# Kernel tuning notes

Measured on AMD Instinct MI355X. Metric: run time of the kernel, lower is better.

The kernel has to match this reference:

```python
import jax, jax.numpy as jnp
import numpy as np

# model_grid_shape (flipped ensemble grid, all equal here); E = 8 experts
GRID = (2, 2, 2)
E = GRID[0] * GRID[1] * GRID[2]
N = 524288   # query points
H = 64       # sub-model MLP hidden width


def setup_inputs() -> dict:
    key = jax.random.key(0)
    ks = jax.random.split(key, 4)
    # query coordinates in [-1, 1]^3
    x = jax.random.uniform(ks[0], (N, 3), jnp.float32, -1.0, 1.0)
    # per-expert spatial extents: axis-aligned cells tiling [-1,1]^3, in the
    # same flat order as the routing index i0 + i1*g0 + i2*g0*g1
    i = np.arange(E)
    cell = np.stack([i % GRID[0], (i // GRID[0]) % GRID[1],
                     i // (GRID[0] * GRID[1])], axis=-1).astype(np.float32)
    g = np.array(GRID, np.float32)
    extents_min = jnp.asarray(-1.0 + 2.0 * cell / g)          # [E, 3]
    extents_max = jnp.asarray(-1.0 + 2.0 * (cell + 1.0) / g)  # [E, 3]
    # per-expert SRN MLP parameters: 3 -> H -> H -> 1
    W1 = jax.random.normal(ks[1], (E, 3, H), jnp.float32) / np.sqrt(3.0)
    b1 = jnp.zeros((E, H), jnp.float32)
    W2 = jax.random.normal(ks[2], (E, H, H), jnp.float32) / np.sqrt(float(H))
    b2 = jnp.zeros((E, H), jnp.float32)
    W3 = jax.random.normal(ks[3], (E, H, 1), jnp.float32) / np.sqrt(float(H))
    b3 = jnp.zeros((E, 1), jnp.float32)
    return {"x": x, "extents_min": extents_min, "extents_max": extents_max,
            "W1": W1, "b1": b1, "W2": W2, "b2": b2, "W3": W3, "b3": b3}


def reference(x, extents_min, extents_max, W1, b1, W2, b2, W3, b3):
    # --- routing: flat expert index per point (matches torch forward) ---
    u = jnp.clip((x + 1.0) * 0.5, 0.0, 0.99)
    gvec = jnp.asarray(GRID, x.dtype)
    gi = (u * gvec).astype(jnp.int32)                       # [N, 3]
    idx = gi[:, 0] + gi[:, 1] * GRID[0] + gi[:, 2] * (GRID[0] * GRID[1])

    # --- dispatch/combine: scan over experts, masked scatter into y ---
    def body(y, args):
        i, emin, emax, w1, bb1, w2, bb2, w3, bb3 = args
        # normalize point into expert-local [-1, 1]^3
        xn = -1.0 + 2.0 * ((x - emin) / (emax - emin))      # [N, 3]
        h = jax.nn.relu(xn @ w1 + bb1)                      # [N, H]
        h = jax.nn.relu(h @ w2 + bb2)                       # [N, H]
        o = h @ w3 + bb3                                    # [N, 1]
        mask = (idx == i)[:, None]
        return jnp.where(mask, o, y), None

    y0 = jnp.zeros((x.shape[0], 1), x.dtype)
    y, _ = jax.lax.scan(
        body, y0,
        (jnp.arange(E), extents_min, extents_max, W1, b1, W2, b2, W3, b3))
    return y
```

## Files before the change

kernel.cpp:

```cpp
#include <hip/hip_runtime.h>

typedef __bf16 bf16x8 __attribute__((ext_vector_type(8)));
typedef float f32x4 __attribute__((ext_vector_type(4)));
typedef unsigned short u16x8 __attribute__((ext_vector_type(8)));

#define N_PTS 524288
#define HBLK 256
#define PTS_PER_HBLK 2048

__device__ __forceinline__ unsigned short f2bf(float f) {
    unsigned u = __float_as_uint(f);
    u += 0x7FFFu + ((u >> 16) & 1u);
    return (unsigned short)(u >> 16);
}

__device__ __forceinline__ int route(float x0, float x1, float x2) {
    int g0 = (int)(fminf(fmaxf((x0 + 1.0f) * 0.5f, 0.0f), 0.99f) * 2.0f);
    int g1 = (int)(fminf(fmaxf((x1 + 1.0f) * 0.5f, 0.0f), 0.99f) * 2.0f);
    int g2 = (int)(fminf(fmaxf((x2 + 1.0f) * 0.5f, 0.0f), 0.99f) * 2.0f);
    return g0 + 2*g1 + 4*g2;
}

#define OFF_HIST  0u
#define OFF_BB    8192u
#define OFF_CNT   16384u
#define OFF_BASE  16416u
#define OFF_W1P   16448u
#define OFF_W2T   24640u
#define OFF_XG    90176u

extern "C" __global__ void __launch_bounds__(256) k1_hist(
        const float* __restrict__ x, int* __restrict__ hist) {
    __shared__ int lh[8];
    int t = threadIdx.x;
    if (t < 8) lh[t] = 0;
    __syncthreads();
    int base = blockIdx.x * PTS_PER_HBLK;
    #pragma unroll
    for (int i = 0; i < 8; ++i) {
        int p = base + i * 256 + t;
        float x0 = x[3*p], x1 = x[3*p+1], x2 = x[3*p+2];
        atomicAdd(&lh[route(x0, x1, x2)], 1);
    }
    __syncthreads();
    if (t < 8) hist[blockIdx.x * 8 + t] = lh[t];
}

extern "C" __global__ void __launch_bounds__(256) k2_prep(
        const float* __restrict__ emin, const float* __restrict__ emax,
        const float* __restrict__ W1, const float* __restrict__ b1,
        const float* __restrict__ W2,
        const int* __restrict__ hist, int* __restrict__ blockBase,
        int* __restrict__ counts, int* __restrict__ bases,
        float4* __restrict__ W1p, unsigned short* __restrict__ W2T) {
    int t = threadIdx.x;
    if (blockIdx.x == 8) {
        __shared__ int lh[256][9];
        int c[8], incl[8];
        #pragma unroll
        for (int e = 0; e < 8; ++e) { c[e] = hist[t*8 + e]; incl[e] = c[e]; lh[t][e] = c[e]; }
        for (int off = 1; off < 256; off <<= 1) {
            __syncthreads();
            int add[8];
            if (t >= off) {
                #pragma unroll
                for (int e = 0; e < 8; ++e) add[e] = lh[t - off][e];
            }
            __syncthreads();
            if (t >= off) {
                #pragma unroll
                for (int e = 0; e < 8; ++e) { incl[e] += add[e]; lh[t][e] = incl[e]; }
            }
        }
        __syncthreads();
        int tot[8], base[8];
        int r = 0;
        #pragma unroll
        for (int e = 0; e < 8; ++e) { tot[e] = lh[255][e]; base[e] = r; r += tot[e]; }
        #pragma unroll
        for (int e = 0; e < 8; ++e) blockBase[t*8 + e] = base[e] + incl[e] - c[e];
        if (t == 0) {
            #pragma unroll
            for (int e = 0; e < 8; ++e) { counts[e] = tot[e]; bases[e] = base[e]; }
        }
    } else {
        int e = blockIdx.x;
        if (t < 64) {
            int n = t;
            float d0 = emax[e*3+0] - emin[e*3+0];
            float d1 = emax[e*3+1] - emin[e*3+1];
            float d2 = emax[e*3+2] - emin[e*3+2];
            float a0 = 2.0f/d0, a1 = 2.0f/d1, a2 = 2.0f/d2;
            float c0 = -1.0f - 2.0f*emin[e*3+0]/d0;
            float c1 = -1.0f - 2.0f*emin[e*3+1]/d1;
            float c2 = -1.0f - 2.0f*emin[e*3+2]/d2;
            float w0 = W1[(e*3+0)*64 + n];
            float w1 = W1[(e*3+1)*64 + n];
            float w2 = W1[(e*3+2)*64 + n];
            float4 w;
            w.x = a0*w0; w.y = a1*w1; w.z = a2*w2;
            w.w = c0*w0 + c1*w1 + c2*w2 + b1[e*64 + n];
            W1p[e*64 + n] = w;
        }
        for (int i = t; i < 4096; i += 256) {
            int k = i >> 6, n = i & 63;
            W2T[e*4096 + n*64 + k] = f2bf(W2[(e*64 + k)*64 + n]);
        }
    }
}

extern "C" __global__ void __launch_bounds__(256) k3_scatter(
        const float* __restrict__ x, const int* __restrict__ blockBase,
        float4* __restrict__ xg) {
    __shared__ int lc[8];
    int t = threadIdx.x;
    int b = blockIdx.x;
    if (t < 8) lc[t] = blockBase[b*8 + t];
    __syncthreads();
    int base = b * PTS_PER_HBLK;
    #pragma unroll
    for (int i = 0; i < 8; ++i) {
        int p = base + i * 256 + t;
        float x0 = x[3*p], x1 = x[3*p+1], x2 = x[3*p+2];
        int e = route(x0, x1, x2);
        int pos = atomicAdd(&lc[e], 1);
        float4 v;
        v.x = x0; v.y = x1; v.z = x2; v.w = __uint_as_float((unsigned)p);
        xg[pos] = v;
    }
}

extern "C" __global__ void __launch_bounds__(256, 3) k4_mlp(
        const float4* __restrict__ xg,
        const int* __restrict__ counts, const int* __restrict__ bases,
        const float4* __restrict__ W1p, const unsigned short* __restrict__ W2T,
        const float* __restrict__ b2, const float* __restrict__ W3,
        const float* __restrict__ b3, float* __restrict__ y) {
    int e = blockIdx.y;
    int cnt = counts[e];
    int tileStart = blockIdx.x * 256;
    if (tileStart >= cnt) return;
    int base = bases[e];

    int t = threadIdx.x;
    int lane = t & 63, wave = t >> 6;
    int m16 = lane & 15;
    int g  = lane >> 4;
    int g8 = g * 8;

    __shared__ __align__(16) unsigned short h1s[256][72];
    __shared__ float4 w1s[64];
    __shared__ float  b2s[64], w3s[64];

    if (t < 64)        w1s[t]       = W1p[e*64 + t];
    else if (t < 128)  b2s[t - 64]  = b2[e*64 + (t - 64)];
    else if (t < 192)  w3s[t - 128] = W3[e*64 + (t - 128)];

    int valid = (tileStart + t) < cnt;
    float px = 0.f, py = 0.f, pz = 0.f;
    unsigned pidx = 0;
    if (valid) {
        float4 v = xg[base + tileStart + t];
        px = v.x; py = v.y; pz = v.z; pidx = __float_as_uint(v.w);
    }
    __syncthreads();

    #pragma unroll
    for (int jb = 0; jb < 8; ++jb) {
        u16x8 hv;
        #pragma unroll
        for (int j2 = 0; j2 < 8; ++j2) {
            float4 w = w1s[jb*8 + j2];
            float h = fmaf(px, w.x, fmaf(py, w.y, fmaf(pz, w.z, w.w)));
            hv[j2] = f2bf(fmaxf(h, 0.0f));
        }
        *(u16x8*)(&h1s[t][jb*8]) = hv;
    }
    __syncthreads();

    const unsigned short* w2e = W2T + e*4096;
    bf16x8 A[4][2];
    #pragma unroll
    for (int mt = 0; mt < 4; ++mt)
        #pragma unroll
        for (int kt = 0; kt < 2; ++kt)
            A[mt][kt] = *(const bf16x8*)(w2e + (mt*16 + m16)*64 + kt*32 + g8);

    f32x4 acc[4][4] = {};
    #pragma unroll
    for (int pt = 0; pt < 4; ++pt) {
        int row = wave*64 + pt*16 + m16;
        bf16x8 B0 = *(const bf16x8*)(&h1s[row][g8]);
        bf16x8 B1 = *(const bf16x8*)(&h1s[row][32 + g8]);
        #pragma unroll
        for (int mt = 0; mt < 4; ++mt) {
            acc[mt][pt] = __builtin_amdgcn_mfma_f32_16x16x32_bf16(A[mt][0], B0, acc[mt][pt], 0, 0, 0);
            acc[mt][pt] = __builtin_amdgcn_mfma_f32_16x16x32_bf16(A[mt][1], B1, acc[mt][pt], 0, 0, 0);
        }
    }

    float bb3 = b3[e];
    #pragma unroll
    for (int pt = 0; pt < 4; ++pt) {
        float s = 0.0f;
        #pragma unroll
        for (int mt = 0; mt < 4; ++mt) {
            #pragma unroll
            for (int r = 0; r < 4; ++r) {
                int f = mt*16 + g*4 + r;
                float h2 = fmaxf(acc[mt][pt][r] + b2s[f], 0.0f);
                s = fmaf(h2, w3s[f], s);
            }
        }
        s += __shfl_xor(s, 16, 64);
        s += __shfl_xor(s, 32, 64);
        unsigned oi = (unsigned)__shfl((int)pidx, pt*16 + m16, 64);
        int row = wave*64 + pt*16 + m16;
        if (lane < 16 && (tileStart + row) < cnt) {
            y[oi] = s + bb3;
        }
    }
}

extern "C" void kernel_launch(void* const* d_in, const int* in_sizes, int n_in,
                              void* d_out, int out_size, void* d_ws, size_t ws_size,
                              hipStream_t stream) {
    const float* x    = (const float*)d_in[0];
    const float* emin = (const float*)d_in[1];
    const float* emax = (const float*)d_in[2];
    const float* W1   = (const float*)d_in[3];
    const float* b1   = (const float*)d_in[4];
    const float* W2   = (const float*)d_in[5];
    const float* b2   = (const float*)d_in[6];
    const float* W3   = (const float*)d_in[7];
    const float* b3   = (const float*)d_in[8];
    float* y = (float*)d_out;

    char* ws = (char*)d_ws;
    int*  hist      = (int*)(ws + OFF_HIST);
    int*  blockBase = (int*)(ws + OFF_BB);
    int*  counts    = (int*)(ws + OFF_CNT);
    int*  bases     = (int*)(ws + OFF_BASE);
    float4* W1p     = (float4*)(ws + OFF_W1P);
    unsigned short* W2T = (unsigned short*)(ws + OFF_W2T);
    float4* xg      = (float4*)(ws + OFF_XG);

    k1_hist<<<HBLK, 256, 0, stream>>>(x, hist);
    k2_prep<<<9, 256, 0, stream>>>(emin, emax, W1, b1, W2, hist, blockBase, counts, bases, W1p, W2T);
    k3_scatter<<<HBLK, 256, 0, stream>>>(x, blockBase, xg);
    k4_mlp<<<dim3(288, 8), 256, 0, stream>>>(xg, counts, bases, W1p, W2T, b2, W3, b3, y);
}
```

Before: 106.0 us.

## Replace histogram-scan-scatter with atomic cursor per-expert bucketing

Removes the separate histogram kernel and the prefix-scan block. The scatter kernel now counts routes locally and claims space in fixed-capacity per-expert buckets with a global atomic on a cursor. This cuts one launch and a second pass over x, but makes the order of points within each bucket nondeterministic. The MLP kernel also reads layer-1 weights directly from global memory instead of LDS, which drops a barrier, and uses a packed float-to-bf16 conversion.

Result: no change. 106.0 us (+0.0%).

```diff
diff --git a/kernel.cpp b/kernel.cpp
--- a/kernel.cpp
+++ b/kernel.cpp
@@ -1,12 +1,14 @@
 #include <hip/hip_runtime.h>
 
 typedef __bf16 bf16x8 __attribute__((ext_vector_type(8)));
+typedef __bf16 bf16x2 __attribute__((ext_vector_type(2)));
 typedef float f32x4 __attribute__((ext_vector_type(4)));
-typedef unsigned short u16x8 __attribute__((ext_vector_type(8)));
+typedef float f32x2 __attribute__((ext_vector_type(2)));
 
 #define N_PTS 524288
-#define HBLK 256
-#define PTS_PER_HBLK 2048
+#define SBLK 256
+#define PTS_PER_SBLK 2048
+#define CAP 524288
 
 __device__ __forceinline__ unsigned short f2bf(float f) {
     unsigned u = __float_as_uint(f);
@@ -21,126 +23,86 @@
     return g0 + 2*g1 + 4*g2;
 }
 
-#define OFF_HIST  0u
-#define OFF_BB    8192u
-#define OFF_CNT   16384u
-#define OFF_BASE  16416u
-#define OFF_W1P   16448u
-#define OFF_W2T   24640u
-#define OFF_XG    90176u
-
-extern "C" __global__ void __launch_bounds__(256) k1_hist(
-        const float* __restrict__ x, int* __restrict__ hist) {
-    __shared__ int lh[8];
-    int t = threadIdx.x;
-    if (t < 8) lh[t] = 0;
-    __syncthreads();
-    int base = blockIdx.x * PTS_PER_HBLK;
-    #pragma unroll
-    for (int i = 0; i < 8; ++i) {
-        int p = base + i * 256 + t;
-        float x0 = x[3*p], x1 = x[3*p+1], x2 = x[3*p+2];
-        atomicAdd(&lh[route(x0, x1, x2)], 1);
-    }
-    __syncthreads();
-    if (t < 8) hist[blockIdx.x * 8 + t] = lh[t];
-}
-
-extern "C" __global__ void __launch_bounds__(256) k2_prep(
+#define OFF_CNT  0u
+#define OFF_W1P  64u
+#define OFF_W2T  8320u
+#define OFF_XG   1048576u
+
+extern "C" __global__ void __launch_bounds__(256) kPrep(
         const float* __restrict__ emin, const float* __restrict__ emax,
         const float* __restrict__ W1, const float* __restrict__ b1,
         const float* __restrict__ W2,
-        const int* __restrict__ hist, int* __restrict__ blockBase,
-        int* __restrict__ counts, int* __restrict__ bases,
-        float4* __restrict__ W1p, unsigned short* __restrict__ W2T) {
+        int* __restrict__ cursor, float4* __restrict__ W1p,
+        unsigned short* __restrict__ W2T) {
     int t = threadIdx.x;
-    if (blockIdx.x == 8) {
-        __shared__ int lh[256][9];
-        int c[8], incl[8];
-        #pragma unroll
-        for (int e = 0; e < 8; ++e) { c[e] = hist[t*8 + e]; incl[e] = c[e]; lh[t][e] = c[e]; }
-        for (int off = 1; off < 256; off <<= 1) {
-            __syncthreads();
-            int add[8];
-            if (t >= off) {
-                #pragma unroll
-                for (int e = 0; e < 8; ++e) add[e] = lh[t - off][e];
-            }
-            __syncthreads();
-            if (t >= off) {
-                #pragma unroll
-                for (int e = 0; e < 8; ++e) { incl[e] += add[e]; lh[t][e] = incl[e]; }
-            }
-        }
-        __syncthreads();
-        int tot[8], base[8];
-        int r = 0;
-        #pragma unroll
-        for (int e = 0; e < 8; ++e) { tot[e] = lh[255][e]; base[e] = r; r += tot[e]; }
-        #pragma unroll
-        for (int e = 0; e < 8; ++e) blockBase[t*8 + e] = base[e] + incl[e] - c[e];
-        if (t == 0) {
-            #pragma unroll
-            for (int e = 0; e < 8; ++e) { counts[e] = tot[e]; bases[e] = base[e]; }
-        }
-    } else {
-        int e = blockIdx.x;
-        if (t < 64) {
-            int n = t;
-            float d0 = emax[e*3+0] - emin[e*3+0];
-            float d1 = emax[e*3+1] - emin[e*3+1];
-            float d2 = emax[e*3+2] - emin[e*3+2];
-            float a0 = 2.0f/d0, a1 = 2.0f/d1, a2 = 2.0f/d2;
-            float c0 = -1.0f - 2.0f*emin[e*3+0]/d0;
-            float c1 = -1.0f - 2.0f*emin[e*3+1]/d1;
-            float c2 = -1.0f - 2.0f*emin[e*3+2]/d2;
-            float w0 = W1[(e*3+0)*64 + n];
-            float w1 = W1[(e*3+1)*64 + n];
-            float w2 = W1[(e*3+2)*64 + n];
-            float4 w;
-            w.x = a0*w0; w.y = a1*w1; w.z = a2*w2;
-            w.w = c0*w0 + c1*w1 + c2*w2 + b1[e*64 + n];
-            W1p[e*64 + n] = w;
-        }
-        for (int i = t; i < 4096; i += 256) {
-            int k = i >> 6, n = i & 63;
-            W2T[e*4096 + n*64 + k] = f2bf(W2[(e*64 + k)*64 + n]);
-        }
+    int e = blockIdx.x;
+    if (e == 0 && t < 8) cursor[t] = 0;
+    if (t < 64) {
+        int n = t;
+        float d0 = emax[e*3+0] - emin[e*3+0];
+        float d1 = emax[e*3+1] - emin[e*3+1];
+        float d2 = emax[e*3+2] - emin[e*3+2];
+        float a0 = 2.0f/d0, a1 = 2.0f/d1, a2 = 2.0f/d2;
+        float c0 = -1.0f - 2.0f*emin[e*3+0]/d0;
+        float c1 = -1.0f - 2.0f*emin[e*3+1]/d1;
+        float c2 = -1.0f - 2.0f*emin[e*3+2]/d2;
+        float w0 = W1[(e*3+0)*64 + n];
+        float w1 = W1[(e*3+1)*64 + n];
+        float w2 = W1[(e*3+2)*64 + n];
+        float4 w;
+        w.x = a0*w0; w.y = a1*w1; w.z = a2*w2;
+        w.w = c0*w0 + c1*w1 + c2*w2 + b1[e*64 + n];
+        W1p[e*64 + n] = w;
+    }
+    for (int i = t; i < 4096; i += 256) {
+        int k = i >> 6, n = i & 63;
+        W2T[e*4096 + n*64 + k] = f2bf(W2[(e*64 + k)*64 + n]);
     }
 }
 
 extern "C" __global__ void __launch_bounds__(256) k3_scatter(
-        const float* __restrict__ x, const int* __restrict__ blockBase,
+        const float* __restrict__ x, int* __restrict__ cursor,
         float4* __restrict__ xg) {
-    __shared__ int lc[8];
+    __shared__ int lh[8];
+    __shared__ int startS[8];
     int t = threadIdx.x;
-    int b = blockIdx.x;
-    if (t < 8) lc[t] = blockBase[b*8 + t];
-    __syncthreads();
-    int base = b * PTS_PER_HBLK;
+    if (t < 8) lh[t] = 0;
+    __syncthreads();
+    int base = blockIdx.x * PTS_PER_SBLK;
+    float c0[8], c1[8], c2[8];
+    unsigned epack = 0;
     #pragma unroll
     for (int i = 0; i < 8; ++i) {
         int p = base + i * 256 + t;
-        float x0 = x[3*p], x1 = x[3*p+1], x2 = x[3*p+2];
-        int e = route(x0, x1, x2);
-        int pos = atomicAdd(&lc[e], 1);
+        c0[i] = x[3*p]; c1[i] = x[3*p+1]; c2[i] = x[3*p+2];
+        int e = route(c0[i], c1[i], c2[i]);
+        epack |= (unsigned)e << (3*i);
+        atomicAdd(&lh[e], 1);
+    }
+    __syncthreads();
+    if (t < 8) { startS[t] = atomicAdd(&cursor[t], lh[t]); lh[t] = 0; }
+    __syncthreads();
+    #pragma unroll
+    for (int i = 0; i < 8; ++i) {
+        int e = (epack >> (3*i)) & 7;
+        int r = atomicAdd(&lh[e], 1);
         float4 v;
-        v.x = x0; v.y = x1; v.z = x2; v.w = __uint_as_float((unsigned)p);
-        xg[pos] = v;
+        v.x = c0[i]; v.y = c1[i]; v.z = c2[i];
+        v.w = __uint_as_float((unsigned)(base + i * 256 + t));
+        xg[e*CAP + startS[e] + r] = v;
     }
 }
 
 extern "C" __global__ void __launch_bounds__(256, 3) k4_mlp(
-        const float4* __restrict__ xg,
-        const int* __restrict__ counts, const int* __restrict__ bases,
+        const float4* __restrict__ xg, const int* __restrict__ cursor,
         const float4* __restrict__ W1p, const unsigned short* __restrict__ W2T,
         const float* __restrict__ b2, const float* __restrict__ W3,
         const float* __restrict__ b3, float* __restrict__ y) {
     int e = blockIdx.y;
-    int cnt = counts[e];
+    int cnt = cursor[e];
     int tileStart = blockIdx.x * 256;
     if (tileStart >= cnt) return;
-    int base = bases[e];
+    int base = e * CAP;
 
     int t = threadIdx.x;
     int lane = t & 63, wave = t >> 6;
@@ -149,12 +111,10 @@
     int g8 = g * 8;
 
     __shared__ __align__(16) unsigned short h1s[256][72];
-    __shared__ float4 w1s[64];
-    __shared__ float  b2s[64], w3s[64];
-
-    if (t < 64)        w1s[t]       = W1p[e*64 + t];
-    else if (t < 128)  b2s[t - 64]  = b2[e*64 + (t - 64)];
-    else if (t < 192)  w3s[t - 128] = W3[e*64 + (t - 128)];
+    __shared__ float b2s[64], w3s[64];
+
+    if (t >= 64 && t < 128)       b2s[t - 64]  = b2[e*64 + (t - 64)];
+    else if (t >= 128 && t < 192) w3s[t - 128] = W3[e*64 + (t - 128)];
 
     int valid = (tileStart + t) < cnt;
     float px = 0.f, py = 0.f, pz = 0.f;
@@ -163,18 +123,24 @@
         float4 v = xg[base + tileStart + t];
         px = v.x; py = v.y; pz = v.z; pidx = __float_as_uint(v.w);
     }
-    __syncthreads();
-
+
+    const float4* __restrict__ w1e = W1p + e * 64;
     #pragma unroll
     for (int jb = 0; jb < 8; ++jb) {
-        u16x8 hv;
-        #pragma unroll
-        for (int j2 = 0; j2 < 8; ++j2) {
-            float4 w = w1s[jb*8 + j2];
-            float h = fmaf(px, w.x, fmaf(py, w.y, fmaf(pz, w.z, w.w)));
-            hv[j2] = f2bf(fmaxf(h, 0.0f));
-        }
-        *(u16x8*)(&h1s[t][jb*8]) = hv;
+        bf16x8 hv;
+        #pragma unroll
+        for (int j2 = 0; j2 < 8; j2 += 2) {
+            float4 wa = w1e[jb*8 + j2];
+            float4 wb = w1e[jb*8 + j2 + 1];
+            float ha = fmaf(px, wa.x, fmaf(py, wa.y, fmaf(pz, wa.z, wa.w)));
+            float hb = fmaf(px, wb.x, fmaf(py, wb.y, fmaf(pz, wb.z, wb.w)));
+            f32x2 hp;
+            hp[0] = fmaxf(ha, 0.0f);
+            hp[1] = fmaxf(hb, 0.0f);
+            bf16x2 bp = __builtin_convertvector(hp, bf16x2);
+            hv[j2] = bp[0]; hv[j2+1] = bp[1];
+        }
+        *(bf16x8*)(&h1s[t][jb*8]) = hv;
     }
     __syncthreads();
 
@@ -237,16 +203,12 @@
     float* y = (float*)d_out;
 
     char* ws = (char*)d_ws;
-    int*  hist      = (int*)(ws + OFF_HIST);
-    int*  blockBase = (int*)(ws + OFF_BB);
-    int*  counts    = (int*)(ws + OFF_CNT);
-    int*  bases     = (int*)(ws + OFF_BASE);
+    int*  cursor    = (int*)(ws + OFF_CNT);
     float4* W1p     = (float4*)(ws + OFF_W1P);
     unsigned short* W2T = (unsigned short*)(ws + OFF_W2T);
     float4* xg      = (float4*)(ws + OFF_XG);
 
-    k1_hist<<<HBLK, 256, 0, stream>>>(x, hist);
-    k2_prep<<<9, 256, 0, stream>>>(emin, emax, W1, b1, W2, hist, blockBase, counts, bases, W1p, W2T);
-    k3_scatter<<<HBLK, 256, 0, stream>>>(x, blockBase, xg);
-    k4_mlp<<<dim3(288, 8), 256, 0, stream>>>(xg, counts, bases, W1p, W2T, b2, W3, b3, y);
-}
+    kPrep<<<8, 256, 0, stream>>>(emin, emax, W1, b1, W2, cursor, W1p, W2T);
+    k3_scatter<<<SBLK, 256, 0, stream>>>(x, cursor, xg);
+    k4_mlp<<<dim3(288, 8), 256, 0, stream>>>(xg, cursor, W1p, W2T, b2, W3, b3, y);
+}
```
